# Kernel optimization log

Hardware: AMD Instinct MI355X
Metric: run time of the kernel (lower is better)

## Reference

```python
import jax, jax.numpy as jnp
import numpy as np

EPS = 1e-6  # torch.nn.PairwiseDistance default eps, added to the difference before norm
B, D, H, W = 2048, 1024, 128, 128


def setup_inputs() -> dict:
    key = jax.random.key(0)
    k1, k2 = jax.random.split(key)
    x = jax.random.normal(k1, (B, D), dtype=jnp.float32)
    # SOM codebook: [input_size, H*W], matches torch.randn(input_size, out_size[0]*out_size[1])
    weight = jax.random.normal(k2, (D, H * W), dtype=jnp.float32)
    # grid locations, row-major (x, y) as produced by get_map_index()
    gx, gy = jnp.meshgrid(jnp.arange(H), jnp.arange(W), indexing='ij')
    locations = jnp.stack([gx.ravel(), gy.ravel()], axis=1).astype(jnp.float32)  # [H*W, 2]
    return {"x": x, "weight": weight, "locations": locations}


def reference(x, weight, locations):
    # dists[b, m] = || x[b] - weight[:, m] + EPS ||_2  (PairwiseDistance p=2 semantics)
    d = x.shape[1]
    sq = (jnp.sum(x * x, axis=1, keepdims=True)          # [B, 1]
          + jnp.sum(weight * weight, axis=0)[None, :]    # [1, M]
          - 2.0 * (x @ weight)                            # [B, M] GEMM
          + 2.0 * EPS * (jnp.sum(x, axis=1, keepdims=True) - jnp.sum(weight, axis=0)[None, :])
          + d * EPS * EPS)
    dists = jnp.sqrt(jnp.maximum(sq, 0.0))                # [B, M]
    losses = jnp.min(dists, axis=1, keepdims=True)        # [B, 1]
    bmu_indexes = jnp.argmin(dists, axis=1, keepdims=True)  # [B, 1] int
    bmu_locations = locations[bmu_indexes]                 # [B, 1, 2]
    loss = jnp.sum(losses) / x.shape[0]                    # scalar mean min-distance
    return bmu_indexes, bmu_locations, loss
```

## Files before the change

kernel.cpp:

```cpp
#include <hip/hip_runtime.h>
#include <cstdint>
#include <cstddef>


#define B_  2048
#define D_  1024
#define M_  16384
#define EPS_ 1e-6f

typedef _Float16 v8h __attribute__((ext_vector_type(8)));
typedef float    v4f __attribute__((ext_vector_type(4)));

static __device__ __forceinline__ unsigned long long umin64(unsigned long long a,
                                                            unsigned long long b) {
    return a < b ? a : b;
}

static __device__ __forceinline__ size_t addr16(int r, int c) {
    return (size_t)(r >> 4) * 32768 + (size_t)(c >> 2) * 1024 +
           (size_t)(c & 3) * 256 + (size_t)(r & 15) * 16;
}

#define GLDS16(g, l)                                                            \
    __builtin_amdgcn_global_load_lds(                                           \
        (const __attribute__((address_space(1))) void*)(g),                     \
        (__attribute__((address_space(3))) void*)(l), 16, 0, 0)

__global__ __launch_bounds__(256) void prep(
    const float* __restrict__ x, const float* __restrict__ W,
    _Float16* __restrict__ xh, _Float16* __restrict__ xl,
    _Float16* __restrict__ wth, _Float16* __restrict__ wtl,
    float* __restrict__ rowTerm, float* __restrict__ colTerm,
    unsigned long long* __restrict__ keys, float* __restrict__ out)
{
    const int t = threadIdx.x;
    const int blk = blockIdx.x;
    if (blk < 256) {
        __shared__ float tile[64][65];
        __shared__ float colsq[64];
        if (t < 64) colsq[t] = 0.f;
        const int m0 = blk * 64;
        const int dloc = t >> 4, mq = (t & 15) * 4;
        const int m_local = t & 63, cp = t >> 6;
        for (int dt = 0; dt < 16; ++dt) {
            const int d0 = dt * 64;
            __syncthreads();
            #pragma unroll
            for (int s = 0; s < 4; ++s) {
                float4 v = *(const float4*)(W + (size_t)(d0 + dloc + 16 * s) * M_ + m0 + mq);
                tile[dloc + 16 * s][mq + 0] = v.x;
                tile[dloc + 16 * s][mq + 1] = v.y;
                tile[dloc + 16 * s][mq + 2] = v.z;
                tile[dloc + 16 * s][mq + 3] = v.w;
            }
            __syncthreads();
            v8h h0, l0, h1, l1;
            float part = 0.f;
            #pragma unroll
            for (int e = 0; e < 8; ++e) {
                float v = tile[16 * cp + e][m_local];
                _Float16 hi = (_Float16)v;
                h0[e] = hi; l0[e] = (_Float16)(v - (float)hi);
                part += v * v - 2.0f * EPS_ * v;
            }
            #pragma unroll
            for (int e = 0; e < 8; ++e) {
                float v = tile[16 * cp + 8 + e][m_local];
                _Float16 hi = (_Float16)v;
                h1[e] = hi; l1[e] = (_Float16)(v - (float)hi);
                part += v * v - 2.0f * EPS_ * v;
            }
            atomicAdd(&colsq[m_local], part);
            const int m  = m0 + m_local;
            const int c0 = dt * 8 + 2 * cp;
            const size_t a0 = addr16(m, c0), a1 = addr16(m, c0 + 1);
            *(v8h*)((char*)wth + a0) = h0; *(v8h*)((char*)wth + a1) = h1;
            *(v8h*)((char*)wtl + a0) = l0; *(v8h*)((char*)wtl + a1) = l1;
        }
        __syncthreads();
        if (t < 64) colTerm[m0 + t] = colsq[t];
    } else if (blk < 320) {
        __shared__ float rsum[2];
        const int rb0 = (blk - 256) * 32;
        for (int p = 0; p < 16; ++p) {
            if (t < 2) rsum[t] = 0.f;
            __syncthreads();
            const int r = rb0 + 2 * p + (t >> 7);
            const int c = t & 127;
            float4 q1 = *(const float4*)(x + (size_t)r * D_ + 8 * c);
            float4 q2 = *(const float4*)(x + (size_t)r * D_ + 8 * c + 4);
            float vv[8] = {q1.x, q1.y, q1.z, q1.w, q2.x, q2.y, q2.z, q2.w};
            v8h h, l;
            float part = 0.f;
            #pragma unroll
            for (int e = 0; e < 8; ++e) {
                _Float16 hi = (_Float16)vv[e];
                h[e] = hi; l[e] = (_Float16)(vv[e] - (float)hi);
                part += vv[e] * vv[e] + 2.0f * EPS_ * vv[e];
            }
            const size_t a = addr16(r, c);
            *(v8h*)((char*)xh + a) = h;
            *(v8h*)((char*)xl + a) = l;
            for (int off = 32; off; off >>= 1) part += __shfl_down(part, off, 64);
            if ((t & 63) == 0) atomicAdd(&rsum[t >> 7], part);
            __syncthreads();
            if ((t & 127) == 0) rowTerm[r] = rsum[t >> 7];
            __syncthreads();
        }
    } else {
        for (int i = t; i < B_; i += 256) keys[i] = ~0ull;
        if (t == 0) out[3 * B_] = 0.f;
    }
}

__global__ __launch_bounds__(256, 2) void som_mfma(
    const _Float16* __restrict__ xh, const _Float16* __restrict__ xl,
    const _Float16* __restrict__ wth, const _Float16* __restrict__ wtl,
    const float* __restrict__ rowTerm, const float* __restrict__ colTerm,
    unsigned long long* __restrict__ keys)
{
    __shared__ __align__(16) char smem[49152];
    _Float16* Ah = (_Float16*)smem;
    _Float16* Al = (_Float16*)(smem + 8192);
    _Float16* Bh = (_Float16*)(smem + 16384);
    _Float16* Bl = (_Float16*)(smem + 32768);

    const int t = threadIdx.x;
    const int g = blockIdx.x;
    const int cb = (g >> 4) * 256;
    const int rb = (g & 15) * 128;
    const int L = t & 63, w = t >> 6;
    const int wro = (w >> 1) * 64;
    const int wco = (w & 1) * 128;
    const int c16 = L & 15, kq = L >> 4;

    const int wgrp = t >> 6;
    const int lane16 = (t & 63) * 16;
    const int ldsw = wgrp * 1024;
    const size_t abase0 = (size_t)((rb >> 4) + wgrp) * 32768 + lane16;
    const size_t abase1 = abase0 + 4ull * 32768;
    const size_t bbase0 = (size_t)((cb >> 4) + wgrp) * 32768 + lane16;
    const size_t bbase1 = bbase0 + 4ull * 32768;
    const size_t bbase2 = bbase0 + 8ull * 32768;
    const size_t bbase3 = bbase0 + 12ull * 32768;

    const char* pxh = (const char*)xh;
    const char* pxl = (const char*)xl;
    const char* pwh = (const char*)wth;
    const char* pwl = (const char*)wtl;

    v4f acc[4][8];
    #pragma unroll
    for (int i = 0; i < 4; ++i)
        #pragma unroll
        for (int j = 0; j < 8; ++j) acc[i][j] = (v4f){0.f, 0.f, 0.f, 0.f};

    const int lofs = kq * 128 + c16 * 8;
    int ia[4], ibx[8];
    #pragma unroll
    for (int i = 0; i < 4; ++i) ia[i] = ((wro >> 4) + i) * 512 + lofs;
    #pragma unroll
    for (int j = 0; j < 8; ++j) ibx[j] = ((wco >> 4) + j) * 512 + lofs;

    for (int S = 0; S < 32; ++S) {
        const size_t ko = (size_t)S * 1024;
        __syncthreads();
        GLDS16(pxh + abase0 + ko, smem + ldsw);
        GLDS16(pxh + abase1 + ko, smem + 4096 + ldsw);
        GLDS16(pxl + abase0 + ko, smem + 8192 + ldsw);
        GLDS16(pxl + abase1 + ko, smem + 12288 + ldsw);
        GLDS16(pwh + bbase0 + ko, smem + 16384 + ldsw);
        GLDS16(pwh + bbase1 + ko, smem + 20480 + ldsw);
        GLDS16(pwh + bbase2 + ko, smem + 24576 + ldsw);
        GLDS16(pwh + bbase3 + ko, smem + 28672 + ldsw);
        GLDS16(pwl + bbase0 + ko, smem + 32768 + ldsw);
        GLDS16(pwl + bbase1 + ko, smem + 36864 + ldsw);
        GLDS16(pwl + bbase2 + ko, smem + 40960 + ldsw);
        GLDS16(pwl + bbase3 + ko, smem + 45056 + ldsw);
        __syncthreads();

        v8h ah[4], al4[4], bh4[4], bl4[4];
        #pragma unroll
        for (int i = 0; i < 4; ++i) {
            ah[i]  = *(const v8h*)(Ah + ia[i]);
            al4[i] = *(const v8h*)(Al + ia[i]);
        }
        #pragma unroll
        for (int j = 0; j < 4; ++j) {
            bh4[j] = *(const v8h*)(Bh + ibx[j]);
            bl4[j] = *(const v8h*)(Bl + ibx[j]);
        }
        #pragma unroll
        for (int i = 0; i < 4; ++i)
            #pragma unroll
            for (int j = 0; j < 4; ++j) {
                acc[i][j] = __builtin_amdgcn_mfma_f32_16x16x32_f16(ah[i],  bh4[j], acc[i][j], 0, 0, 0);
                acc[i][j] = __builtin_amdgcn_mfma_f32_16x16x32_f16(ah[i],  bl4[j], acc[i][j], 0, 0, 0);
                acc[i][j] = __builtin_amdgcn_mfma_f32_16x16x32_f16(al4[i], bh4[j], acc[i][j], 0, 0, 0);
            }
        #pragma unroll
        for (int j = 0; j < 4; ++j) {
            bh4[j] = *(const v8h*)(Bh + ibx[j + 4]);
            bl4[j] = *(const v8h*)(Bl + ibx[j + 4]);
        }
        #pragma unroll
        for (int i = 0; i < 4; ++i)
            #pragma unroll
            for (int j = 0; j < 4; ++j) {
                acc[i][j+4] = __builtin_amdgcn_mfma_f32_16x16x32_f16(ah[i],  bh4[j], acc[i][j+4], 0, 0, 0);
                acc[i][j+4] = __builtin_amdgcn_mfma_f32_16x16x32_f16(ah[i],  bl4[j], acc[i][j+4], 0, 0, 0);
                acc[i][j+4] = __builtin_amdgcn_mfma_f32_16x16x32_f16(al4[i], bh4[j], acc[i][j+4], 0, 0, 0);
            }
    }

    float cT[8];
    #pragma unroll
    for (int j = 0; j < 8; ++j) cT[j] = colTerm[cb + wco + j * 16 + c16];
    const float de2 = (float)D_ * EPS_ * EPS_;
    #pragma unroll
    for (int i = 0; i < 4; ++i) {
        #pragma unroll
        for (int r = 0; r < 4; ++r) {
            int row_g = rb + wro + i * 16 + kq * 4 + r;
            float rt = rowTerm[row_g];
            unsigned long long best = ~0ull;
            #pragma unroll
            for (int j = 0; j < 8; ++j) {
                float sq = rt + cT[j] - 2.0f * acc[i][j][r] + de2;
                sq = fmaxf(sq, 0.0f);
                float dist = sqrtf(sq);
                unsigned long long key =
                    ((unsigned long long)__float_as_uint(dist) << 32) |
                    (unsigned int)(cb + wco + j * 16 + c16);
                best = umin64(best, key);
            }
            #pragma unroll
            for (int m = 1; m <= 8; m <<= 1) {
                unsigned long long o =
                    (unsigned long long)__shfl_xor((long long)best, m, 64);
                best = umin64(best, o);
            }
            if (c16 == 0) atomicMin(&keys[row_g], best);
        }
    }
}

__global__ void row_stats(const float* __restrict__ x, float* __restrict__ rowTerm) {
    int b = blockIdx.x;
    const float* xr = x + (size_t)b * D_;
    int t = threadIdx.x;
    float acc = 0.f;
    for (int i = t; i < D_; i += 256) {
        float v = xr[i];
        acc += v * v + 2.0f * EPS_ * v;
    }
    for (int off = 32; off; off >>= 1) acc += __shfl_down(acc, off, 64);
    __shared__ float s[4];
    if ((t & 63) == 0) s[t >> 6] = acc;
    __syncthreads();
    if (t == 0) rowTerm[b] = s[0] + s[1] + s[2] + s[3];
}

__global__ void col_stats(const float* __restrict__ w, float* __restrict__ colTerm) {
    int m = blockIdx.x * 256 + threadIdx.x;
    int d0 = blockIdx.y * 64;
    const float* p = w + (size_t)d0 * M_ + m;
    float acc = 0.f;
    #pragma unroll 8
    for (int d = 0; d < 64; ++d) {
        float v = p[(size_t)d * M_];
        acc += v * v - 2.0f * EPS_ * v;
    }
    atomicAdd(&colTerm[m], acc);
}

__global__ __launch_bounds__(256, 2) void som_gemm(
    const float* __restrict__ A, const float* __restrict__ Wt,
    const float* __restrict__ rowTerm, const float* __restrict__ colTerm,
    unsigned long long* __restrict__ keys)
{
    __shared__ float As[8][128];
    __shared__ float Bs[8][128];
    const int t  = threadIdx.x;
    const int rb = blockIdx.y * 128;
    const int cb = blockIdx.x * 128;
    const int tx = t & 15;
    const int ty = t >> 4;
    float acc[8][8];
    #pragma unroll
    for (int i = 0; i < 8; ++i)
        #pragma unroll
        for (int j = 0; j < 8; ++j) acc[i][j] = 0.f;
    const int la_row = t >> 1, la_k = (t & 1) * 4;
    const int lb_k = t >> 5, lb_n = (t & 31) * 4;
    const float* Aptr = A + (size_t)(rb + la_row) * D_ + la_k;
    const float* Bptr = Wt + (size_t)lb_k * M_ + cb + lb_n;
    for (int k0 = 0; k0 < D_; k0 += 8) {
        float4 av = *(const float4*)(Aptr + k0);
        float4 bv = *(const float4*)(Bptr + (size_t)k0 * M_);
        __syncthreads();
        As[la_k + 0][la_row] = av.x;
        As[la_k + 1][la_row] = av.y;
        As[la_k + 2][la_row] = av.z;
        As[la_k + 3][la_row] = av.w;
        *(float4*)&Bs[lb_k][lb_n] = bv;
        __syncthreads();
        #pragma unroll
        for (int k = 0; k < 8; ++k) {
            float a[8], b[8];
            #pragma unroll
            for (int i = 0; i < 8; ++i) a[i] = As[k][ty * 8 + i];
            #pragma unroll
            for (int j = 0; j < 8; ++j) b[j] = Bs[k][tx * 8 + j];
            #pragma unroll
            for (int i = 0; i < 8; ++i)
                #pragma unroll
                for (int j = 0; j < 8; ++j) acc[i][j] += a[i] * b[j];
        }
    }
    float rT[8], cT[8];
    #pragma unroll
    for (int i = 0; i < 8; ++i) rT[i] = rowTerm[rb + ty * 8 + i];
    #pragma unroll
    for (int j = 0; j < 8; ++j) cT[j] = colTerm[cb + tx * 8 + j];
    const float de2 = (float)D_ * EPS_ * EPS_;
    #pragma unroll
    for (int i = 0; i < 8; ++i) {
        unsigned long long best = ~0ull;
        #pragma unroll
        for (int j = 0; j < 8; ++j) {
            float sq = rT[i] + cT[j] - 2.0f * acc[i][j] + de2;
            sq = fmaxf(sq, 0.0f);
            float dist = sqrtf(sq);
            unsigned long long key =
                ((unsigned long long)__float_as_uint(dist) << 32) |
                (unsigned int)(cb + tx * 8 + j);
            best = umin64(best, key);
        }
        #pragma unroll
        for (int msk = 1; msk <= 8; msk <<= 1) {
            unsigned long long o = __shfl_xor((long long)best, msk, 64);
            best = umin64(best, (unsigned long long)o);
        }
        if (tx == 0) atomicMin(&keys[rb + ty * 8 + i], best);
    }
}

__global__ void finalize(const unsigned long long* __restrict__ keys,
                         const float* __restrict__ loc,
                         float* __restrict__ out)
{
    int t = threadIdx.x;
    int r = blockIdx.x * 256 + t;
    unsigned long long k = keys[r];
    unsigned int idx = (unsigned int)(k & 0xFFFFFFFFu);
    float dist = __uint_as_float((unsigned int)(k >> 32));
    out[r] = (float)idx;
    out[B_ + 2 * r]     = loc[2 * idx];
    out[B_ + 2 * r + 1] = loc[2 * idx + 1];
    float sum = dist;
    for (int off = 32; off; off >>= 1) sum += __shfl_down(sum, off, 64);
    __shared__ float s[4];
    if ((t & 63) == 0) s[t >> 6] = sum;
    __syncthreads();
    if (t == 0) atomicAdd(&out[3 * B_], (s[0] + s[1] + s[2] + s[3]) / (float)B_);
}

extern "C" void kernel_launch(void* const* d_in, const int* in_sizes, int n_in,
                              void* d_out, int out_size, void* d_ws, size_t ws_size,
                              hipStream_t stream)
{
    const float* x   = (const float*)d_in[0];
    const float* w   = (const float*)d_in[1];
    const float* loc = (const float*)d_in[2];
    float* out = (float*)d_out;

    char* ws = (char*)d_ws;
    unsigned long long* keys = (unsigned long long*)ws;
    float* rowTerm = (float*)(ws + (16 << 10));
    float* colTerm = (float*)(ws + (24 << 10));
    _Float16* xh  = (_Float16*)(ws + (1ull << 20));
    _Float16* xl  = (_Float16*)(ws + (5ull << 20));
    _Float16* wth = (_Float16*)(ws + (9ull << 20));
    _Float16* wtl = (_Float16*)(ws + (41ull << 20));
    const size_t NEED = 73ull << 20;

    if (ws_size >= NEED) {
        prep<<<321, 256, 0, stream>>>(x, w, xh, xl, wth, wtl,
                                      rowTerm, colTerm, keys, out);
        som_mfma<<<1024, 256, 0, stream>>>(
            xh, xl, wth, wtl, rowTerm, colTerm, keys);
    } else {
        hipMemsetAsync(keys, 0xFF, B_ * sizeof(unsigned long long), stream);
        hipMemsetAsync(colTerm, 0, M_ * sizeof(float), stream);
        hipMemsetAsync(out + 3 * B_, 0, sizeof(float), stream);
        row_stats<<<B_, 256, 0, stream>>>(x, rowTerm);
        col_stats<<<dim3(M_ / 256, D_ / 64), 256, 0, stream>>>(w, colTerm);
        som_gemm<<<dim3(M_ / 128, B_ / 128), 256, 0, stream>>>(
            x, w, rowTerm, colTerm, keys);
    }
    finalize<<<8, 256, 0, stream>>>(keys, loc, out);
}
```

Baseline: 310.9 us.

## Parallelize weight prep over D, fuse finalize into GEMM, defer sqrt

The prep kernel now splits the weight conversion across 8 D-slices (2048 blocks instead of 256), writing partial column sums that the GEMM epilogue adds up. The row-prep part also gets more, smaller blocks. The finalize launch is folded into som_mfma: a last-block-done counter lets the final block gather the argmin keys, write indexes and locations, and compute the mean loss. Keys compare squared distances, so sqrt runs only in that final pass. Occupancy hint rises to 3 blocks per CU. The trade-offs are a serialized tail in one block and register pressure from the tighter launch bound.

Result: slower. 815.4 us (+162.2%).

```diff
diff --git a/kernel.cpp b/kernel.cpp
--- a/kernel.cpp
+++ b/kernel.cpp
@@ -30,20 +30,22 @@
     const float* __restrict__ x, const float* __restrict__ W,
     _Float16* __restrict__ xh, _Float16* __restrict__ xl,
     _Float16* __restrict__ wth, _Float16* __restrict__ wtl,
-    float* __restrict__ rowTerm, float* __restrict__ colTerm,
-    unsigned long long* __restrict__ keys, float* __restrict__ out)
+    float* __restrict__ rowTerm, float* __restrict__ colPart,
+    unsigned long long* __restrict__ keys, unsigned int* __restrict__ cnt,
+    float* __restrict__ out)
 {
     const int t = threadIdx.x;
     const int blk = blockIdx.x;
-    if (blk < 256) {
+    if (blk < 2048) {
         __shared__ float tile[64][65];
-        __shared__ float colsq[64];
-        if (t < 64) colsq[t] = 0.f;
-        const int m0 = blk * 64;
+        const int m0 = (blk & 255) * 64;
+        const int d0base = (blk >> 8) * 128;
         const int dloc = t >> 4, mq = (t & 15) * 4;
-        const int m_local = t & 63, cp = t >> 6;
-        for (int dt = 0; dt < 16; ++dt) {
-            const int d0 = dt * 64;
+        const int mloc = t >> 2, j = t & 3;
+        const int dc = j * 16;
+        float part = 0.f;
+        for (int half = 0; half < 2; ++half) {
+            const int d0 = d0base + half * 64;
             __syncthreads();
             #pragma unroll
             for (int s = 0; s < 4; ++s) {
@@ -55,34 +57,33 @@
             }
             __syncthreads();
             v8h h0, l0, h1, l1;
-            float part = 0.f;
             #pragma unroll
             for (int e = 0; e < 8; ++e) {
-                float v = tile[16 * cp + e][m_local];
+                float v = tile[dc + e][mloc];
                 _Float16 hi = (_Float16)v;
                 h0[e] = hi; l0[e] = (_Float16)(v - (float)hi);
                 part += v * v - 2.0f * EPS_ * v;
             }
             #pragma unroll
             for (int e = 0; e < 8; ++e) {
-                float v = tile[16 * cp + 8 + e][m_local];
+                float v = tile[dc + 8 + e][mloc];
                 _Float16 hi = (_Float16)v;
                 h1[e] = hi; l1[e] = (_Float16)(v - (float)hi);
                 part += v * v - 2.0f * EPS_ * v;
             }
-            atomicAdd(&colsq[m_local], part);
-            const int m  = m0 + m_local;
-            const int c0 = dt * 8 + 2 * cp;
+            const int m  = m0 + mloc;
+            const int c0 = (d0 >> 3) + j * 2;
             const size_t a0 = addr16(m, c0), a1 = addr16(m, c0 + 1);
             *(v8h*)((char*)wth + a0) = h0; *(v8h*)((char*)wth + a1) = h1;
             *(v8h*)((char*)wtl + a0) = l0; *(v8h*)((char*)wtl + a1) = l1;
         }
-        __syncthreads();
-        if (t < 64) colTerm[m0 + t] = colsq[t];
-    } else if (blk < 320) {
+        part += __shfl_xor(part, 1, 64);
+        part += __shfl_xor(part, 2, 64);
+        if (j == 0) colPart[(blk >> 8) * M_ + m0 + mloc] = part;
+    } else if (blk < 2304) {
         __shared__ float rsum[2];
-        const int rb0 = (blk - 256) * 32;
-        for (int p = 0; p < 16; ++p) {
+        const int rb0 = (blk - 2048) * 8;
+        for (int p = 0; p < 4; ++p) {
             if (t < 2) rsum[t] = 0.f;
             __syncthreads();
             const int r = rb0 + 2 * p + (t >> 7);
@@ -109,15 +110,16 @@
         }
     } else {
         for (int i = t; i < B_; i += 256) keys[i] = ~0ull;
-        if (t == 0) out[3 * B_] = 0.f;
-    }
-}
-
-__global__ __launch_bounds__(256, 2) void som_mfma(
+        if (t == 0) { *cnt = 0u; out[3 * B_] = 0.f; }
+    }
+}
+
+__global__ __launch_bounds__(256, 3) void som_mfma(
     const _Float16* __restrict__ xh, const _Float16* __restrict__ xl,
     const _Float16* __restrict__ wth, const _Float16* __restrict__ wtl,
-    const float* __restrict__ rowTerm, const float* __restrict__ colTerm,
-    unsigned long long* __restrict__ keys)
+    const float* __restrict__ rowTerm, const float* __restrict__ colPart,
+    unsigned long long* __restrict__ keys, unsigned int* __restrict__ cnt,
+    const float* __restrict__ loc, float* __restrict__ out)
 {
     __shared__ __align__(16) char smem[49152];
     _Float16* Ah = (_Float16*)smem;
@@ -215,7 +217,13 @@
 
     float cT[8];
     #pragma unroll
-    for (int j = 0; j < 8; ++j) cT[j] = colTerm[cb + wco + j * 16 + c16];
+    for (int j = 0; j < 8; ++j) {
+        const int col = cb + wco + j * 16 + c16;
+        float s = 0.f;
+        #pragma unroll
+        for (int p = 0; p < 8; ++p) s += colPart[p * M_ + col];
+        cT[j] = s;
+    }
     const float de2 = (float)D_ * EPS_ * EPS_;
     #pragma unroll
     for (int i = 0; i < 4; ++i) {
@@ -228,9 +236,8 @@
             for (int j = 0; j < 8; ++j) {
                 float sq = rt + cT[j] - 2.0f * acc[i][j][r] + de2;
                 sq = fmaxf(sq, 0.0f);
-                float dist = sqrtf(sq);
                 unsigned long long key =
-                    ((unsigned long long)__float_as_uint(dist) << 32) |
+                    ((unsigned long long)__float_as_uint(sq) << 32) |
                     (unsigned int)(cb + wco + j * 16 + c16);
                 best = umin64(best, key);
             }
@@ -242,6 +249,33 @@
             }
             if (c16 == 0) atomicMin(&keys[row_g], best);
         }
+    }
+
+    __threadfence();
+    __shared__ int lastFlag;
+    if (t == 0) {
+        unsigned int old = atomicAdd(cnt, 1u);
+        lastFlag = (old == (unsigned int)(gridDim.x - 1));
+    }
+    __syncthreads();
+    if (lastFlag) {
+        __threadfence();
+        float sum = 0.f;
+        for (int r = t; r < B_; r += 256) {
+            unsigned long long k = atomicMin(&keys[r], ~0ull);
+            unsigned int idx = (unsigned int)(k & 0xFFFFFFFFu);
+            float sqv = __uint_as_float((unsigned int)(k >> 32));
+            float dist = sqrtf(sqv);
+            out[r] = (float)idx;
+            out[B_ + 2 * r]     = loc[2 * idx];
+            out[B_ + 2 * r + 1] = loc[2 * idx + 1];
+            sum += dist;
+        }
+        for (int off = 32; off; off >>= 1) sum += __shfl_down(sum, off, 64);
+        __shared__ float sred[4];
+        if ((t & 63) == 0) sred[t >> 6] = sum;
+        __syncthreads();
+        if (t == 0) out[3 * B_] = (sred[0] + sred[1] + sred[2] + sred[3]) / (float)B_;
     }
 }
 
@@ -378,7 +412,8 @@
     char* ws = (char*)d_ws;
     unsigned long long* keys = (unsigned long long*)ws;
     float* rowTerm = (float*)(ws + (16 << 10));
-    float* colTerm = (float*)(ws + (24 << 10));
+    unsigned int* cnt = (unsigned int*)(ws + (24 << 10));
+    float* colPart = (float*)(ws + (32 << 10));
     _Float16* xh  = (_Float16*)(ws + (1ull << 20));
     _Float16* xl  = (_Float16*)(ws + (5ull << 20));
     _Float16* wth = (_Float16*)(ws + (9ull << 20));
@@ -386,11 +421,12 @@
     const size_t NEED = 73ull << 20;
 
     if (ws_size >= NEED) {
-        prep<<<321, 256, 0, stream>>>(x, w, xh, xl, wth, wtl,
-                                      rowTerm, colTerm, keys, out);
+        prep<<<2305, 256, 0, stream>>>(x, w, xh, xl, wth, wtl,
+                                       rowTerm, colPart, keys, cnt, out);
         som_mfma<<<1024, 256, 0, stream>>>(
-            xh, xl, wth, wtl, rowTerm, colTerm, keys);
+            xh, xl, wth, wtl, rowTerm, colPart, keys, cnt, loc, out);
     } else {
+        float* colTerm = (float*)(ws + (32 << 10));
         hipMemsetAsync(keys, 0xFF, B_ * sizeof(unsigned long long), stream);
         hipMemsetAsync(colTerm, 0, M_ * sizeof(float), stream);
         hipMemsetAsync(out + 3 * B_, 0, sizeof(float), stream);
@@ -398,6 +434,6 @@
         col_stats<<<dim3(M_ / 256, D_ / 64), 256, 0, stream>>>(w, colTerm);
         som_gemm<<<dim3(M_ / 128, B_ / 128), 256, 0, stream>>>(
             x, w, rowTerm, colTerm, keys);
-    }
-    finalize<<<8, 256, 0, stream>>>(keys, loc, out);
-}
+        finalize<<<8, 256, 0, stream>>>(keys, loc, out);
+    }
+}
```
